# Kernel optimization log

Hardware: AMD Instinct MI355X
Metric: run time of the kernel (lower is better)

The kernel has to match this reference:

```python
import jax, jax.numpy as jnp
import numpy as np

B, STATE_DIM, MLP_DIM, H, W = 128, 64, 512, 40, 40
LN_EPS = 1e-5


def _sobel_kernel(c):
    # Per-channel depthwise filters in torch order: [c0_sx, c0_sy, c0_id, c1_sx, ...]
    sx = jnp.array([[-1., 0., 1.], [-2., 0., 2.], [-1., 0., 1.]], jnp.float32)
    sy = jnp.array([[-1., -2., -1.], [0., 0., 0.], [1., 2., 1.]], jnp.float32)
    ident = jnp.array([[0., 0., 0.], [0., 1., 0.], [0., 0., 0.]], jnp.float32)
    k = jnp.stack([sx, sy, ident])[:, None]      # [3, 1, 3, 3]
    return jnp.tile(k, (c, 1, 1, 1))             # [3c, 1, 3, 3]


def setup_inputs() -> dict:
    key = jax.random.key(0)
    ks = jax.random.split(key, 6)
    state_in = jax.random.normal(ks[0], (B, STATE_DIM, H, W), jnp.float32)
    w1 = jax.random.normal(ks[1], (MLP_DIM, 3 * STATE_DIM), jnp.float32) * 0.05
    ln_weight = jax.random.uniform(ks[2], (MLP_DIM, H, W), jnp.float32, 0.5, 1.5)
    ln_bias = jax.random.normal(ks[3], (MLP_DIM, H, W), jnp.float32) * 0.01
    w2 = jax.random.normal(ks[4], (STATE_DIM, MLP_DIM), jnp.float32) * 0.05
    mask = jax.random.randint(ks[5], (H, W), 0, 2, jnp.int32)  # bernoulli(0.5) update mask
    return {"state_in": state_in, "w1": w1, "ln_weight": ln_weight,
            "ln_bias": ln_bias, "w2": w2, "mask": mask}


def reference(state_in, w1, ln_weight, ln_bias, w2, mask):
    C = state_in.shape[1]
    # Depthwise 3x3 sobel/identity perception: [B, C, H, W] -> [B, 3C, H, W]
    kern = _sobel_kernel(C)
    x = jax.lax.conv_general_dilated(
        state_in, kern, window_strides=(1, 1), padding='SAME',
        dimension_numbers=('NCHW', 'OIHW', 'NCHW'), feature_group_count=C)
    # 1x1 conv (no bias): [B, 3C, H, W] -> [B, MLP, H, W]
    x = jnp.einsum('bchw,oc->bohw', x, w1)
    # LayerNorm over (MLP, H, W) per sample, with elementwise affine
    mu = jnp.mean(x, axis=(1, 2, 3), keepdims=True)
    var = jnp.var(x, axis=(1, 2, 3), keepdims=True)
    x = (x - mu) * jax.lax.rsqrt(var + LN_EPS) * ln_weight + ln_bias
    x = jax.nn.relu(x)
    # 1x1 conv back to state channels (zero-init in original; random here for testing)
    x = jnp.einsum('bchw,oc->bohw', x, w2)
    # Stochastic per-pixel update mask, broadcast over batch and channels
    x = x * mask.astype(jnp.float32)
    # Alive mask: 3x3 max-pool on alive channel, stride 1, SAME padding
    live = jax.lax.reduce_window(state_in[:, 3], -jnp.inf, jax.lax.max,
                                 (1, 3, 3), (1, 1, 1), 'SAME')
    live = (live > 0.1).astype(jnp.float32)[:, None]  # [B, 1, H, W]
    return state_in + x * live
```

## Files before the change

kernel.cpp:

```cpp
#include <hip/hip_runtime.h>


typedef unsigned short u16;
typedef unsigned int   u32;
typedef __attribute__((ext_vector_type(8))) u16    ushort8;
typedef __attribute__((ext_vector_type(4))) u16    u16x4;
typedef __attribute__((ext_vector_type(8))) __bf16 bf16x8;
typedef __attribute__((ext_vector_type(4))) float  f32x4;
typedef __attribute__((ext_vector_type(4))) u32    u32x4;

#define NB   128
#define NC   64
#define K1   192
#define NO   512
#define NHW  1600
#define LN_N 819200.0f

__device__ __forceinline__ u16 f2bf(float f) {
    union { __bf16 h; u16 u; } v; v.h = (__bf16)f; return v.u;
}
__device__ __forceinline__ float bf2f(u16 h) {
    union { u32 u; float f; } v; v.u = ((u32)h) << 16; return v.f;
}
__device__ __forceinline__ float bfhi(u32 c) {
    union { u32 u; float f; } v; v.u = c & 0xffff0000u; return v.f;
}
__device__ __forceinline__ float bflo(u32 c) {
    union { u32 u; float f; } v; v.u = c << 16; return v.f;
}
__device__ __forceinline__ f32x4 mfma16(bf16x8 a, bf16x8 b, f32x4 c) {
    return __builtin_amdgcn_mfma_f32_16x16x32_bf16(a, b, c, 0, 0, 0);
}
__device__ __forceinline__ bf16x8 ldfrag(const u16* p) {
    return *(const bf16x8*)p;
}

__device__ __forceinline__ void load_halo(const float* __restrict__ base, int h,
                                          int wq, float reg[3][12]) {
#pragma unroll
    for (int jj = 0; jj < 3; ++jj) {
        int hh = h + jj - 1;
        bool vh = (unsigned)hh < 40u;
        const float* rowp = base + hh * 40;
#pragma unroll
        for (int i = 0; i < 12; ++i) {
            int col = wq * 10 - 1 + i;
            reg[jj][i] = (vh && (unsigned)col < 40u) ? rowp[col] : 0.0f;
        }
    }
}
__device__ __forceinline__ void sobel_px(const float reg[3][12], int t,
                                         float& sx, float& sy, float& idn) {
    sx = (reg[0][t + 2] - reg[0][t]) + 2.0f * (reg[1][t + 2] - reg[1][t])
       + (reg[2][t + 2] - reg[2][t]);
    sy = (reg[2][t] + 2.0f * reg[2][t + 1] + reg[2][t + 2])
       - (reg[0][t] + 2.0f * reg[0][t + 1] + reg[0][t + 2]);
    idn = reg[1][t + 1];
}

__global__ __launch_bounds__(256) void k0_convert(const float* __restrict__ w1,
                                                  const float* __restrict__ w2,
                                                  u16* __restrict__ w1p,
                                                  u16* __restrict__ w1T,
                                                  u16* __restrict__ w2p,
                                                  float* __restrict__ stats) {
    int g = blockIdx.x * 256 + threadIdx.x;
    if (g < NO * K1) {
        u16 v = f2bf(w1[g]);
        int o = g / K1, k = g - o * K1;
        int f = o >> 4, ks = k >> 5;
        int lane = (((k >> 3) & 3) << 4) | (o & 15);
        w1p[(size_t)(((f * 6 + ks) * 64 + lane) * 8 + (k & 7))] = v;
        w1T[(size_t)k * NO + o] = v;
    } else if (g < NO * K1 + NC * NO) {
        int i = g - NO * K1;
        int s = i / NO, o = i - s * NO;
        u16 v = f2bf(w2[i]);
        int wid = s >> 4, oc = o >> 6, ks2 = (o >> 5) & 1;
        int lane = (((o >> 3) & 3) << 4) | (s & 15);
        w2p[(size_t)((((wid * 8 + oc) * 2 + ks2) * 64 + lane) * 8 + (o & 7))] = v;
    } else if (g < NO * K1 + NC * NO + 256) {
        stats[g - NO * K1 - NC * NO] = 0.0f;
    }
}

__global__ __launch_bounds__(256) void k0_lncomb(const float* __restrict__ lnw,
                                                 const float* __restrict__ lnb,
                                                 u32* __restrict__ lnp) {
    int g = blockIdx.x * 256 + threadIdx.x;
    int o = g / NHW, p = g - o * NHW;
    int bx = p / 80, pr = p - bx * 80;
    int mi = pr >> 4, l15 = pr & 15;
    int oc = o >> 6, ro = o & 63;
    int wid = ro >> 4, hi = (ro >> 2) & 3, r = ro & 3;
    int lane = (hi << 4) | l15;
    int outi = ((((bx * 8 + oc) * 4 + wid) * 5 + mi) << 8) + lane * 4 + r;
    lnp[outi] = ((u32)f2bf(lnb[g]) << 16) | f2bf(lnw[g]);
}

__global__ __launch_bounds__(256) void k0_gram(const u16* __restrict__ w1T,
                                               float* __restrict__ G,
                                               float* __restrict__ colw1) {
    const int blk = blockIdx.x;
    const int tid = threadIdx.x;
    const int lane = tid & 63, wid = tid >> 6;
    const int q = lane >> 4, l15 = lane & 15;
    if (blk < 36) {
        int bj = blk / 6, bk = blk - bj * 6;
        int j0 = bj * 32 + (wid & 1) * 16, k0 = bk * 32 + (wid >> 1) * 16;
        f32x4 acc = {0.f, 0.f, 0.f, 0.f};
#pragma unroll
        for (int ks = 0; ks < 16; ++ks) {
            bf16x8 a  = ldfrag(&w1T[(size_t)(j0 + l15) * NO + ks * 32 + q * 8]);
            bf16x8 bb = ldfrag(&w1T[(size_t)(k0 + l15) * NO + ks * 32 + q * 8]);
            acc = mfma16(a, bb, acc);
        }
#pragma unroll
        for (int r = 0; r < 4; ++r)
            G[(size_t)(j0 + q * 4 + r) * K1 + k0 + l15] = acc[r];
    } else if (tid < K1) {
        float s = 0.f;
        for (int i = 0; i < NO / 8; ++i) {
            ushort8 v = *(const ushort8*)&w1T[(size_t)tid * NO + i * 8];
#pragma unroll
            for (int j = 0; j < 8; ++j) s += bf2f(v[j]);
        }
        colw1[tid] = s;
    }
}

__global__ __launch_bounds__(256) void k2_stats(const float* __restrict__ state,
                                                const float* __restrict__ G,
                                                const float* __restrict__ colw1,
                                                float* __restrict__ stats) {
    const int bx = blockIdx.x;
    const int b  = blockIdx.y;
    const int h0 = bx * 2;
    const int tid = threadIdx.x;
    const int lane = tid & 63, wid = tid >> 6;
    const int q = lane >> 4, l15 = lane & 15;
    const int j0 = (wid & 1) * 96, j1 = (wid >> 1) * 96, jo = wid * 48;

    __shared__ __align__(16) u16 Pt[193 * 104];
    __shared__ float red[8];

    for (int i = tid; i < 193 * 104 / 8; i += 256) ((u32x4*)Pt)[i] = (u32x4){0,0,0,0};
    __syncthreads();
    if (tid < 80) Pt[192 * 104 + tid] = 0x3F80u;

    {
        const int c = tid >> 2, wq = tid & 3;
        const float* base = state + ((size_t)b * NC + c) * NHW;
        for (int rr = 0; rr < 2; ++rr) {
            float reg[3][12];
            load_halo(base, h0 + rr, wq, reg);
#pragma unroll
            for (int t = 0; t < 10; ++t) {
                float sx, sy, idn; sobel_px(reg, t, sx, sy, idn);
                int px = rr * 40 + wq * 10 + t;
                Pt[(3 * c + 0) * 104 + px] = f2bf(sx);
                Pt[(3 * c + 1) * 104 + px] = f2bf(sy);
                Pt[(3 * c + 2) * 104 + px] = f2bf(idn);
            }
        }
    }
    __syncthreads();

    float ssq = 0.f;
#pragma unroll 1
    for (int fi = 0; fi < 6; ++fi) {
        f32x4 acc[6];
#pragma unroll
        for (int j = 0; j < 6; ++j) { f32x4 z = {0.f,0.f,0.f,0.f}; acc[j] = z; }
#pragma unroll
        for (int ks = 0; ks < 3; ++ks) {
            bf16x8 av = ldfrag(&Pt[(j0 + fi * 16 + l15) * 104 + ks * 32 + q * 8]);
#pragma unroll
            for (int fj = 0; fj < 6; ++fj) {
                bf16x8 bv = ldfrag(&Pt[(j1 + fj * 16 + l15) * 104 + ks * 32 + q * 8]);
                acc[fj] = mfma16(av, bv, acc[fj]);
            }
        }
#pragma unroll
        for (int fj = 0; fj < 6; ++fj) {
            f32x4 gv = *(const f32x4*)&G[(size_t)(j1 + fj * 16 + l15) * K1
                                         + j0 + fi * 16 + q * 4];
#pragma unroll
            for (int r = 0; r < 4; ++r) ssq += acc[fj][r] * gv[r];
        }
    }

    f32x4 accO[3];
#pragma unroll
    for (int j = 0; j < 3; ++j) { f32x4 z = {0.f,0.f,0.f,0.f}; accO[j] = z; }
#pragma unroll
    for (int ks = 0; ks < 3; ++ks) {
        bf16x8 ao = ldfrag(&Pt[192 * 104 + ks * 32 + q * 8]);
#pragma unroll
        for (int fj = 0; fj < 3; ++fj) {
            bf16x8 bo = ldfrag(&Pt[(jo + fj * 16 + l15) * 104 + ks * 32 + q * 8]);
            accO[fj] = mfma16(ao, bo, accO[fj]);
        }
    }
    float sm = 0.f;
    if (q == 0) {
#pragma unroll
        for (int fj = 0; fj < 3; ++fj)
            sm += accO[fj][0] * colw1[jo + fj * 16 + l15];
    }

#pragma unroll
    for (int off = 32; off > 0; off >>= 1) {
        ssq += __shfl_down(ssq, off);
        sm  += __shfl_down(sm, off);
    }
    if (lane == 0) { red[wid] = ssq; red[4 + wid] = sm; }
    __syncthreads();
    if (tid == 0) {
        atomicAdd(&stats[b * 2],     red[4] + red[5] + red[6] + red[7]);
        atomicAdd(&stats[b * 2 + 1], red[0] + red[1] + red[2] + red[3]);
    }
}

__global__ __launch_bounds__(256, 3) void k4_fused(const float* __restrict__ state,
                                                   const u16* __restrict__ w1p,
                                                   const u16* __restrict__ w2p,
                                                   const u32* __restrict__ lnp,
                                                   const int* __restrict__ mask,
                                                   const float* __restrict__ stats,
                                                   float* __restrict__ out) {
    const int bx = blockIdx.x;
    const int b  = blockIdx.y;
    const int p0 = bx * 80, h0 = bx * 2;
    const int tid = threadIdx.x;
    const int lane = tid & 63, wid = tid >> 6;
    const int q = lane >> 4, l15 = lane & 15;

    __shared__ __align__(16) u16 Pt[80 * 192];
    __shared__ __align__(16) u16 Ys[80 * 64];

    const float s_sum = stats[2 * b], s_sq = stats[2 * b + 1];
    const float inv = 1.0f / LN_N;
    const float mu = s_sum * inv;
    const float var = s_sq * inv - mu * mu;
    const float rs = rsqrtf(var + 1e-5f);
    const float murs = mu * rs;

    {
        const int c = tid >> 2, wq = tid & 3;
        const float* base = state + ((size_t)b * NC + c) * NHW;
        for (int rr = 0; rr < 2; ++rr) {
            float reg[3][12];
            load_halo(base, h0 + rr, wq, reg);
#pragma unroll
            for (int t = 0; t < 10; ++t) {
                float sx, sy, idn; sobel_px(reg, t, sx, sy, idn);
                int px = rr * 40 + wq * 10 + t;
                int k = 3 * c;
#pragma unroll
                for (int i = 0; i < 3; ++i) {
                    int kk = k + i, u = kk >> 3;
                    int elem = px * 192 + (((u & 0x18) | ((u ^ px) & 7)) << 3) + (kk & 7);
                    Pt[elem] = f2bf(i == 0 ? sx : (i == 1 ? sy : idn));
                }
            }
        }
    }
    float g5[5];
    {
        const float* st3 = state + ((size_t)b * NC + 3) * NHW;
#pragma unroll
        for (int mi = 0; mi < 5; ++mi) {
            int p = p0 + mi * 16 + l15;
            int h = p / 40, w = p - h * 40;
            float mx = -1e30f;
#pragma unroll
            for (int dh = -1; dh <= 1; ++dh) {
                int hh = h + dh;
                if ((unsigned)hh < 40u)
#pragma unroll
                    for (int dw = -1; dw <= 1; ++dw) {
                        int wc = w + dw;
                        if ((unsigned)wc < 40u) mx = fmaxf(mx, st3[hh * 40 + wc]);
                    }
            }
            g5[mi] = (mx > 0.1f && mask[p] != 0) ? 1.0f : 0.0f;
        }
    }

    int pB0[5], pB1[5], yR0[5], yR1[5], yW[5];
    {
        const int q8 = q << 3;
        const int wu = wid * 2 + (q >> 1);
#pragma unroll
        for (int mi = 0; mi < 5; ++mi) {
            int r  = mi * 16 + l15;
            int xr = (r & 7) << 3;
            pB0[mi] = r * 192 + (q8 ^ xr);
            pB1[mi] = r * 192 + ((q8 + 32) ^ xr);
            int px = r & 7;
            yR0[mi] = r * 64 + ((q ^ px) << 3);
            yR1[mi] = r * 64 + (((q + 4) ^ px) << 3);
            yW[mi]  = r * 64 + ((wu ^ px) << 3) + (q & 1) * 4;
        }
    }

    bf16x8 a_cur[6];
    {
        const u16* w1base0 = w1p + ((size_t)(0 * 4 + wid) * 6) * 512 + lane * 8;
#pragma unroll
        for (int ks = 0; ks < 6; ++ks) a_cur[ks] = ldfrag(w1base0 + ks * 512);
    }
    __syncthreads();

    f32x4 acc2[5];
#pragma unroll
    for (int i = 0; i < 5; ++i) { f32x4 z = {0.f,0.f,0.f,0.f}; acc2[i] = z; }

    for (int oc = 0; oc < 8; ++oc) {
        u32x4 lv[5];
        {
            const u32* lb = lnp + ((((size_t)bx * 8 + oc) * 4 + wid) * 5) * 256 + lane * 4;
#pragma unroll
            for (int mi = 0; mi < 5; ++mi)
                lv[mi] = *(const u32x4*)(lb + mi * 256);
        }
        const u16* w2base = w2p + ((size_t)(wid * 8 + oc) * 2) * 512 + lane * 8;
        bf16x8 aw0 = ldfrag(w2base);
        bf16x8 aw1 = ldfrag(w2base + 512);

        const u16* w1next = w1p + ((size_t)((((oc + 1) & 7) * 4 + wid) * 6)) * 512
                          + lane * 8;
        f32x4 acc1[5];
#pragma unroll
        for (int i = 0; i < 5; ++i) { f32x4 z = {0.f,0.f,0.f,0.f}; acc1[i] = z; }
#pragma unroll
        for (int ks = 0; ks < 6; ++ks) {
            bf16x8 a = a_cur[ks];
            a_cur[ks] = ldfrag(w1next + ks * 512);
#pragma unroll
            for (int mi = 0; mi < 5; ++mi) {
                int off = ((ks & 1) ? pB1[mi] : pB0[mi]) + (ks >> 1) * 64;
                acc1[mi] = mfma16(a, ldfrag(&Pt[off]), acc1[mi]);
            }
        }
#pragma unroll
        for (int mi = 0; mi < 5; ++mi) {
            u16x4 yv;
#pragma unroll
            for (int r = 0; r < 4; ++r) {
                u32 cc = lv[mi][r];
                float t = fmaf(acc1[mi][r], rs, -murs);
                float y = fmaxf(fmaf(t, bflo(cc), bfhi(cc)), 0.0f);
                yv[r] = f2bf(y);
            }
            *(u16x4*)&Ys[yW[mi]] = yv;
        }
        __syncthreads();
#pragma unroll
        for (int ks2 = 0; ks2 < 2; ++ks2) {
            bf16x8 aw = ks2 ? aw1 : aw0;
#pragma unroll
            for (int mi = 0; mi < 5; ++mi) {
                int off = ks2 ? yR1[mi] : yR0[mi];
                acc2[mi] = mfma16(aw, ldfrag(&Ys[off]), acc2[mi]);
            }
        }
        __syncthreads();
    }

#pragma unroll
    for (int mi = 0; mi < 5; ++mi) {
        int p = p0 + mi * 16 + l15;
        float g = g5[mi];
#pragma unroll
        for (int r = 0; r < 4; ++r) {
            int s = wid * 16 + q * 4 + r;
            size_t idx = ((size_t)b * NC + s) * NHW + p;
            out[idx] = state[idx] + g * acc2[mi][r];
        }
    }
}

extern "C" void kernel_launch(void* const* d_in, const int* in_sizes, int n_in,
                              void* d_out, int out_size, void* d_ws, size_t ws_size,
                              hipStream_t stream) {
    const float* state = (const float*)d_in[0];
    const float* w1    = (const float*)d_in[1];
    const float* lnw   = (const float*)d_in[2];
    const float* lnb   = (const float*)d_in[3];
    const float* w2    = (const float*)d_in[4];
    const int*   mask  = (const int*)d_in[5];
    float* out = (float*)d_out;

    char* ws = (char*)d_ws;
    u16*    w1p   = (u16*)(ws + 0ull);
    u16*    w2p   = (u16*)(ws + 196608ull);
    u32*    lnp   = (u32*)(ws + 262144ull);
    u16*    w1T   = (u16*)(ws + 3538944ull);
    float*  G     = (float*)(ws + 3735552ull);
    float*  colw1 = (float*)(ws + 3883008ull);
    float*  stats = (float*)(ws + 3883776ull);

    k0_convert <<<513, 256, 0, stream>>>(w1, w2, w1p, w1T, w2p, stats);
    k0_lncomb  <<<3200, 256, 0, stream>>>(lnw, lnb, lnp);
    k0_gram    <<<37, 256, 0, stream>>>(w1T, G, colw1);
    k2_stats   <<<dim3(20, 128), 256, 0, stream>>>(state, G, colw1, stats);
    k4_fused   <<<dim3(20, 128), 256, 0, stream>>>(state, w1p, w2p, lnp,
                                                   mask, stats, out);
}
```

Measured before the change: 292.9 us.

## Split second GEMM by K across waves to remove per-chunk block barriers

Each wave now writes its own slice of the hidden activations to a private LDS region and immediately runs the second GEMM over all 64 output channels on that slice, accumulating partial sums. This removes the two __syncthreads per output-channel chunk in the main loop. A final LDS reduction across the four waves then adds up the partials and applies the masks. In exchange each thread holds four times as many accumulators, so launch bounds drop from 3 to 2 blocks per CU, and the epilogue adds extra barriers and LDS traffic.

```diff
diff --git a/kernel.cpp b/kernel.cpp
--- a/kernel.cpp
+++ b/kernel.cpp
@@ -62,7 +62,7 @@
                                                   const float* __restrict__ w2,
                                                   u16* __restrict__ w1p,
                                                   u16* __restrict__ w1T,
-                                                  u16* __restrict__ w2p,
+                                                  u16* __restrict__ w2h,
                                                   float* __restrict__ stats) {
     int g = blockIdx.x * 256 + threadIdx.x;
     if (g < NO * K1) {
@@ -76,9 +76,11 @@
         int i = g - NO * K1;
         int s = i / NO, o = i - s * NO;
         u16 v = f2bf(w2[i]);
-        int wid = s >> 4, oc = o >> 6, ks2 = (o >> 5) & 1;
-        int lane = (((o >> 3) & 3) << 4) | (s & 15);
-        w2p[(size_t)((((wid * 8 + oc) * 2 + ks2) * 64 + lane) * 8 + (o & 7))] = v;
+        int oc = o >> 6, w = (o >> 4) & 3, kk = o & 15;
+        int q = kk >> 3, j = kk & 7;
+        int st = s >> 4, l15 = s & 15;
+        int lane = q * 16 + l15;
+        w2h[(size_t)((((oc * 4 + w) * 4 + st) * 32 + lane) * 8 + j)] = v;
     } else if (g < NO * K1 + NC * NO + 256) {
         stats[g - NO * K1 - NC * NO] = 0.0f;
     }
@@ -222,9 +224,9 @@
     }
 }
 
-__global__ __launch_bounds__(256, 3) void k4_fused(const float* __restrict__ state,
+__global__ __launch_bounds__(256, 2) void k4_fused(const float* __restrict__ state,
                                                    const u16* __restrict__ w1p,
-                                                   const u16* __restrict__ w2p,
+                                                   const u16* __restrict__ w2h,
                                                    const u32* __restrict__ lnp,
                                                    const int* __restrict__ mask,
                                                    const float* __restrict__ stats,
@@ -237,7 +239,8 @@
     const int q = lane >> 4, l15 = lane & 15;
 
     __shared__ __align__(16) u16 Pt[80 * 192];
-    __shared__ __align__(16) u16 Ys[80 * 64];
+    __shared__ __align__(16) u16 Ysw[4 * 80 * 32];
+    __shared__ float g_lds[80];
 
     const float s_sum = stats[2 * b], s_sq = stats[2 * b + 1];
     const float inv = 1.0f / LN_N;
@@ -266,8 +269,15 @@
             }
         }
     }
-    float g5[5];
-    {
+    for (int i = tid; i < 640; i += 256) {
+        int u = i & 1;
+        int row = i >> 1;
+        int w_ = (row * 13108) >> 20;
+        int p  = row - w_ * 80;
+        int unit = (2 + u) ^ (p & 3);
+        *(u32x4*)&Ysw[row * 32 + unit * 8] = (u32x4){0, 0, 0, 0};
+    }
+    if (wid == 0) {
         const float* st3 = state + ((size_t)b * NC + 3) * NHW;
 #pragma unroll
         for (int mi = 0; mi < 5; ++mi) {
@@ -284,26 +294,26 @@
                         if ((unsigned)wc < 40u) mx = fmaxf(mx, st3[hh * 40 + wc]);
                     }
             }
-            g5[mi] = (mx > 0.1f && mask[p] != 0) ? 1.0f : 0.0f;
-        }
-    }
-
-    int pB0[5], pB1[5], yR0[5], yR1[5], yW[5];
+            float g = (mx > 0.1f && mask[p] != 0) ? 1.0f : 0.0f;
+            if (q == 0) g_lds[mi * 16 + l15] = g;
+        }
+    }
+
+    int pB0[5], pB1[5];
     {
         const int q8 = q << 3;
-        const int wu = wid * 2 + (q >> 1);
 #pragma unroll
         for (int mi = 0; mi < 5; ++mi) {
             int r  = mi * 16 + l15;
             int xr = (r & 7) << 3;
             pB0[mi] = r * 192 + (q8 ^ xr);
             pB1[mi] = r * 192 + ((q8 + 32) ^ xr);
-            int px = r & 7;
-            yR0[mi] = r * 64 + ((q ^ px) << 3);
-            yR1[mi] = r * 64 + (((q + 4) ^ px) << 3);
-            yW[mi]  = r * 64 + ((wu ^ px) << 3) + (q & 1) * 4;
-        }
-    }
+        }
+    }
+    const int p3 = l15 & 3;
+    const int ybase = (wid * 80 + l15) * 32;
+    const int wsw = ((((q >> 1) ^ p3) << 3) + (q & 1) * 4);
+    const int rsw = ((q ^ p3) << 3);
 
     bf16x8 a_cur[6];
     {
@@ -313,9 +323,11 @@
     }
     __syncthreads();
 
-    f32x4 acc2[5];
-#pragma unroll
-    for (int i = 0; i < 5; ++i) { f32x4 z = {0.f,0.f,0.f,0.f}; acc2[i] = z; }
+    f32x4 acc2w[4][5];
+#pragma unroll
+    for (int st = 0; st < 4; ++st)
+#pragma unroll
+        for (int mi = 0; mi < 5; ++mi) { f32x4 z = {0.f,0.f,0.f,0.f}; acc2w[st][mi] = z; }
 
     for (int oc = 0; oc < 8; ++oc) {
         u32x4 lv[5];
@@ -325,10 +337,14 @@
             for (int mi = 0; mi < 5; ++mi)
                 lv[mi] = *(const u32x4*)(lb + mi * 256);
         }
-        const u16* w2base = w2p + ((size_t)(wid * 8 + oc) * 2) * 512 + lane * 8;
-        bf16x8 aw0 = ldfrag(w2base);
-        bf16x8 aw1 = ldfrag(w2base + 512);
-
+        bf16x8 awq[4];
+        {
+            const u16* w2base = w2h + ((size_t)((oc * 4 + wid) * 4) * 32) * 8
+                              + (size_t)(lane & 31) * 8;
+#pragma unroll
+            for (int st = 0; st < 4; ++st)
+                awq[st] = ldfrag(w2base + st * 256);
+        }
         const u16* w1next = w1p + ((size_t)((((oc + 1) & 7) * 4 + wid) * 6)) * 512
                           + lane * 8;
         f32x4 acc1[5];
@@ -354,31 +370,39 @@
                 float y = fmaxf(fmaf(t, bflo(cc), bfhi(cc)), 0.0f);
                 yv[r] = f2bf(y);
             }
-            *(u16x4*)&Ys[yW[mi]] = yv;
-        }
+            *(u16x4*)&Ysw[ybase + mi * 512 + wsw] = yv;
+        }
+        bf16x8 bfr[5];
+#pragma unroll
+        for (int mi = 0; mi < 5; ++mi)
+            bfr[mi] = ldfrag(&Ysw[ybase + mi * 512 + rsw]);
+#pragma unroll
+        for (int st = 0; st < 4; ++st)
+#pragma unroll
+            for (int mi = 0; mi < 5; ++mi)
+                acc2w[st][mi] = mfma16(awq[st], bfr[mi], acc2w[st][mi]);
+    }
+
+    __syncthreads();
+    float* R = (float*)Pt;
+    for (int st = 0; st < 4; ++st) {
+#pragma unroll
+        for (int mi = 0; mi < 5; ++mi)
+#pragma unroll
+            for (int r = 0; r < 4; ++r)
+                R[wid * 1280 + (q * 4 + r) * 80 + mi * 16 + l15] = acc2w[st][mi][r];
         __syncthreads();
 #pragma unroll
-        for (int ks2 = 0; ks2 < 2; ++ks2) {
-            bf16x8 aw = ks2 ? aw1 : aw0;
-#pragma unroll
-            for (int mi = 0; mi < 5; ++mi) {
-                int off = ks2 ? yR1[mi] : yR0[mi];
-                acc2[mi] = mfma16(aw, ldfrag(&Ys[off]), acc2[mi]);
-            }
+        for (int e = 0; e < 5; ++e) {
+            int i = e * 256 + tid;
+            int s16 = (i * 13108) >> 20;
+            int p = i - s16 * 80;
+            float sum = R[i] + R[1280 + i] + R[2560 + i] + R[3840 + i];
+            float g = g_lds[p];
+            size_t idx = ((size_t)b * NC + st * 16 + s16) * NHW + p0 + p;
+            out[idx] = state[idx] + g * sum;
         }
         __syncthreads();
-    }
-
-#pragma unroll
-    for (int mi = 0; mi < 5; ++mi) {
-        int p = p0 + mi * 16 + l15;
-        float g = g5[mi];
-#pragma unroll
-        for (int r = 0; r < 4; ++r) {
-            int s = wid * 16 + q * 4 + r;
-            size_t idx = ((size_t)b * NC + s) * NHW + p;
-            out[idx] = state[idx] + g * acc2[mi][r];
-        }
     }
 }
 
@@ -395,17 +419,17 @@
 
     char* ws = (char*)d_ws;
     u16*    w1p   = (u16*)(ws + 0ull);
-    u16*    w2p   = (u16*)(ws + 196608ull);
+    u16*    w2h   = (u16*)(ws + 196608ull);
     u32*    lnp   = (u32*)(ws + 262144ull);
     u16*    w1T   = (u16*)(ws + 3538944ull);
     float*  G     = (float*)(ws + 3735552ull);
     float*  colw1 = (float*)(ws + 3883008ull);
     float*  stats = (float*)(ws + 3883776ull);
 
-    k0_convert <<<513, 256, 0, stream>>>(w1, w2, w1p, w1T, w2p, stats);
+    k0_convert <<<513, 256, 0, stream>>>(w1, w2, w1p, w1T, w2h, stats);
     k0_lncomb  <<<3200, 256, 0, stream>>>(lnw, lnb, lnp);
     k0_gram    <<<37, 256, 0, stream>>>(w1T, G, colw1);
     k2_stats   <<<dim3(20, 128), 256, 0, stream>>>(state, G, colw1, stats);
-    k4_fused   <<<dim3(20, 128), 256, 0, stream>>>(state, w1p, w2p, lnp,
+    k4_fused   <<<dim3(20, 128), 256, 0, stream>>>(state, w1p, w2h, lnp,
                                                    mask, stats, out);
 }
```

New measurement: 370.4 us. 26.4% more time.

## Merge weight-prep kernels into one launch and compute mean via per-thread sums

Applied to the files above, without the earlier changes.

Folds the three preprocessing kernels (weight conversion, LN param packing, Gram/colsum) into a single launch. The Gram and column-sum blocks now read w1 directly instead of an intermediate transposed copy, which removes the w1T buffer and the ordering dependency between kernels. In the stats kernel, the ones-row MFMA used for the mean is replaced by per-thread sums of the sobel outputs, dotted with colw1. The Gram blocks now do strided, uncoalesced fp32 loads of w1, which may slow that part.

```diff
diff --git a/kernel.cpp b/kernel.cpp
--- a/kernel.cpp
+++ b/kernel.cpp
@@ -58,74 +58,74 @@
     idn = reg[1][t + 1];
 }
 
-__global__ __launch_bounds__(256) void k0_convert(const float* __restrict__ w1,
-                                                  const float* __restrict__ w2,
-                                                  u16* __restrict__ w1p,
-                                                  u16* __restrict__ w1T,
-                                                  u16* __restrict__ w2p,
-                                                  float* __restrict__ stats) {
-    int g = blockIdx.x * 256 + threadIdx.x;
-    if (g < NO * K1) {
-        u16 v = f2bf(w1[g]);
-        int o = g / K1, k = g - o * K1;
-        int f = o >> 4, ks = k >> 5;
-        int lane = (((k >> 3) & 3) << 4) | (o & 15);
-        w1p[(size_t)(((f * 6 + ks) * 64 + lane) * 8 + (k & 7))] = v;
-        w1T[(size_t)k * NO + o] = v;
-    } else if (g < NO * K1 + NC * NO) {
-        int i = g - NO * K1;
-        int s = i / NO, o = i - s * NO;
-        u16 v = f2bf(w2[i]);
-        int wid = s >> 4, oc = o >> 6, ks2 = (o >> 5) & 1;
-        int lane = (((o >> 3) & 3) << 4) | (s & 15);
-        w2p[(size_t)((((wid * 8 + oc) * 2 + ks2) * 64 + lane) * 8 + (o & 7))] = v;
-    } else if (g < NO * K1 + NC * NO + 256) {
-        stats[g - NO * K1 - NC * NO] = 0.0f;
-    }
-}
-
-__global__ __launch_bounds__(256) void k0_lncomb(const float* __restrict__ lnw,
-                                                 const float* __restrict__ lnb,
-                                                 u32* __restrict__ lnp) {
-    int g = blockIdx.x * 256 + threadIdx.x;
-    int o = g / NHW, p = g - o * NHW;
-    int bx = p / 80, pr = p - bx * 80;
-    int mi = pr >> 4, l15 = pr & 15;
-    int oc = o >> 6, ro = o & 63;
-    int wid = ro >> 4, hi = (ro >> 2) & 3, r = ro & 3;
-    int lane = (hi << 4) | l15;
-    int outi = ((((bx * 8 + oc) * 4 + wid) * 5 + mi) << 8) + lane * 4 + r;
-    lnp[outi] = ((u32)f2bf(lnb[g]) << 16) | f2bf(lnw[g]);
-}
-
-__global__ __launch_bounds__(256) void k0_gram(const u16* __restrict__ w1T,
-                                               float* __restrict__ G,
-                                               float* __restrict__ colw1) {
-    const int blk = blockIdx.x;
+__global__ __launch_bounds__(256) void k0_all(const float* __restrict__ w1,
+                                              const float* __restrict__ w2,
+                                              const float* __restrict__ lnw,
+                                              const float* __restrict__ lnb,
+                                              u16* __restrict__ w1p,
+                                              u16* __restrict__ w2p,
+                                              u32* __restrict__ lnp,
+                                              float* __restrict__ G,
+                                              float* __restrict__ colw1,
+                                              float* __restrict__ stats) {
+    const int bid = blockIdx.x;
     const int tid = threadIdx.x;
-    const int lane = tid & 63, wid = tid >> 6;
-    const int q = lane >> 4, l15 = lane & 15;
-    if (blk < 36) {
+    if (bid < 513) {
+        int g = bid * 256 + tid;
+        if (g < NO * K1) {
+            u16 v = f2bf(w1[g]);
+            int o = g / K1, k = g - o * K1;
+            int f = o >> 4, ks = k >> 5;
+            int lane = (((k >> 3) & 3) << 4) | (o & 15);
+            w1p[(size_t)(((f * 6 + ks) * 64 + lane) * 8 + (k & 7))] = v;
+        } else if (g < NO * K1 + NC * NO) {
+            int i = g - NO * K1;
+            int s = i / NO, o = i - s * NO;
+            u16 v = f2bf(w2[i]);
+            int wid = s >> 4, oc = o >> 6, ks2 = (o >> 5) & 1;
+            int lane = (((o >> 3) & 3) << 4) | (s & 15);
+            w2p[(size_t)((((wid * 8 + oc) * 2 + ks2) * 64 + lane) * 8 + (o & 7))] = v;
+        } else if (g < NO * K1 + NC * NO + 256) {
+            stats[g - NO * K1 - NC * NO] = 0.0f;
+        }
+    } else if (bid < 3713) {
+        int g = (bid - 513) * 256 + tid;
+        int o = g / NHW, p = g - o * NHW;
+        int bx = p / 80, pr = p - bx * 80;
+        int mi = pr >> 4, l15 = pr & 15;
+        int oc = o >> 6, ro = o & 63;
+        int wid = ro >> 4, hi = (ro >> 2) & 3, r = ro & 3;
+        int lane = (hi << 4) | l15;
+        int outi = ((((bx * 8 + oc) * 4 + wid) * 5 + mi) << 8) + lane * 4 + r;
+        lnp[outi] = ((u32)f2bf(lnb[g]) << 16) | f2bf(lnw[g]);
+    } else if (bid < 3749) {
+        const int blk = bid - 3713;
+        const int lane = tid & 63, wid = tid >> 6;
+        const int q = lane >> 4, l15 = lane & 15;
         int bj = blk / 6, bk = blk - bj * 6;
         int j0 = bj * 32 + (wid & 1) * 16, k0 = bk * 32 + (wid >> 1) * 16;
         f32x4 acc = {0.f, 0.f, 0.f, 0.f};
-#pragma unroll
         for (int ks = 0; ks < 16; ++ks) {
-            bf16x8 a  = ldfrag(&w1T[(size_t)(j0 + l15) * NO + ks * 32 + q * 8]);
-            bf16x8 bb = ldfrag(&w1T[(size_t)(k0 + l15) * NO + ks * 32 + q * 8]);
-            acc = mfma16(a, bb, acc);
+            union { u16 u[8]; bf16x8 v; } A, B;
+#pragma unroll
+            for (int j = 0; j < 8; ++j) {
+                int o = ks * 32 + q * 8 + j;
+                A.u[j] = f2bf(w1[(size_t)o * K1 + j0 + l15]);
+                B.u[j] = f2bf(w1[(size_t)o * K1 + k0 + l15]);
+            }
+            acc = mfma16(A.v, B.v, acc);
         }
 #pragma unroll
         for (int r = 0; r < 4; ++r)
             G[(size_t)(j0 + q * 4 + r) * K1 + k0 + l15] = acc[r];
-    } else if (tid < K1) {
-        float s = 0.f;
-        for (int i = 0; i < NO / 8; ++i) {
-            ushort8 v = *(const ushort8*)&w1T[(size_t)tid * NO + i * 8];
-#pragma unroll
-            for (int j = 0; j < 8; ++j) s += bf2f(v[j]);
-        }
-        colw1[tid] = s;
+    } else {
+        if (tid < K1) {
+            float s = 0.f;
+#pragma unroll 8
+            for (int o = 0; o < NO; ++o)
+                s += bf2f(f2bf(w1[(size_t)o * K1 + tid]));
+            colw1[tid] = s;
+        }
     }
 }
 
@@ -139,17 +139,17 @@
     const int tid = threadIdx.x;
     const int lane = tid & 63, wid = tid >> 6;
     const int q = lane >> 4, l15 = lane & 15;
-    const int j0 = (wid & 1) * 96, j1 = (wid >> 1) * 96, jo = wid * 48;
-
-    __shared__ __align__(16) u16 Pt[193 * 104];
+    const int j0 = (wid & 1) * 96, j1 = (wid >> 1) * 96;
+
+    __shared__ __align__(16) u16 Pt[192 * 104];
     __shared__ float red[8];
 
-    for (int i = tid; i < 193 * 104 / 8; i += 256) ((u32x4*)Pt)[i] = (u32x4){0,0,0,0};
+    for (int i = tid; i < 192 * 104 / 8; i += 256) ((u32x4*)Pt)[i] = (u32x4){0,0,0,0};
     __syncthreads();
-    if (tid < 80) Pt[192 * 104 + tid] = 0x3F80u;
-
-    {
-        const int c = tid >> 2, wq = tid & 3;
+
+    float psum0 = 0.f, psum1 = 0.f, psum2 = 0.f;
+    const int c = tid >> 2, wq = tid & 3;
+    {
         const float* base = state + ((size_t)b * NC + c) * NHW;
         for (int rr = 0; rr < 2; ++rr) {
             float reg[3][12];
@@ -158,12 +158,16 @@
             for (int t = 0; t < 10; ++t) {
                 float sx, sy, idn; sobel_px(reg, t, sx, sy, idn);
                 int px = rr * 40 + wq * 10 + t;
-                Pt[(3 * c + 0) * 104 + px] = f2bf(sx);
-                Pt[(3 * c + 1) * 104 + px] = f2bf(sy);
-                Pt[(3 * c + 2) * 104 + px] = f2bf(idn);
-            }
-        }
-    }
+                u16 v0 = f2bf(sx), v1 = f2bf(sy), v2 = f2bf(idn);
+                Pt[(3 * c + 0) * 104 + px] = v0;
+                Pt[(3 * c + 1) * 104 + px] = v1;
+                Pt[(3 * c + 2) * 104 + px] = v2;
+                psum0 += bf2f(v0); psum1 += bf2f(v1); psum2 += bf2f(v2);
+            }
+        }
+    }
+    float sm = psum0 * colw1[3 * c] + psum1 * colw1[3 * c + 1]
+             + psum2 * colw1[3 * c + 2];
     __syncthreads();
 
     float ssq = 0.f;
@@ -188,25 +192,6 @@
 #pragma unroll
             for (int r = 0; r < 4; ++r) ssq += acc[fj][r] * gv[r];
         }
-    }
-
-    f32x4 accO[3];
-#pragma unroll
-    for (int j = 0; j < 3; ++j) { f32x4 z = {0.f,0.f,0.f,0.f}; accO[j] = z; }
-#pragma unroll
-    for (int ks = 0; ks < 3; ++ks) {
-        bf16x8 ao = ldfrag(&Pt[192 * 104 + ks * 32 + q * 8]);
-#pragma unroll
-        for (int fj = 0; fj < 3; ++fj) {
-            bf16x8 bo = ldfrag(&Pt[(jo + fj * 16 + l15) * 104 + ks * 32 + q * 8]);
-            accO[fj] = mfma16(ao, bo, accO[fj]);
-        }
-    }
-    float sm = 0.f;
-    if (q == 0) {
-#pragma unroll
-        for (int fj = 0; fj < 3; ++fj)
-            sm += accO[fj][0] * colw1[jo + fj * 16 + l15];
     }
 
 #pragma unroll
@@ -397,15 +382,13 @@
     u16*    w1p   = (u16*)(ws + 0ull);
     u16*    w2p   = (u16*)(ws + 196608ull);
     u32*    lnp   = (u32*)(ws + 262144ull);
-    u16*    w1T   = (u16*)(ws + 3538944ull);
     float*  G     = (float*)(ws + 3735552ull);
     float*  colw1 = (float*)(ws + 3883008ull);
     float*  stats = (float*)(ws + 3883776ull);
 
-    k0_convert <<<513, 256, 0, stream>>>(w1, w2, w1p, w1T, w2p, stats);
-    k0_lncomb  <<<3200, 256, 0, stream>>>(lnw, lnb, lnp);
-    k0_gram    <<<37, 256, 0, stream>>>(w1T, G, colw1);
-    k2_stats   <<<dim3(20, 128), 256, 0, stream>>>(state, G, colw1, stats);
-    k4_fused   <<<dim3(20, 128), 256, 0, stream>>>(state, w1p, w2p, lnp,
-                                                   mask, stats, out);
-}
+    k0_all  <<<3750, 256, 0, stream>>>(w1, w2, lnw, lnb, w1p, w2p, lnp,
+                                       G, colw1, stats);
+    k2_stats<<<dim3(20, 128), 256, 0, stream>>>(state, G, colw1, stats);
+    k4_fused<<<dim3(20, 128), 256, 0, stream>>>(state, w1p, w2p, lnp,
+                                                mask, stats, out);
+}
```

Result: slower. 306.9 us (+4.8%).
